# Optimization experiments

Hardware: AMD Instinct MI355X
Metric: run time of the kernel (lower is better)

## Reference

```python
import jax, jax.numpy as jnp
import numpy as np

N_NODES = 50000
IN_DIM = 128
OUT_DIM = 128
N_EDGES = 800000


def setup_inputs() -> dict:
    key = jax.random.key(0)
    k1, k2, k3, k4 = jax.random.split(key, 4)
    h = jax.random.normal(k1, (N_NODES, IN_DIM), dtype=jnp.float32)
    edges = jax.random.randint(k2, (2, N_EDGES), 0, N_NODES, dtype=jnp.int64)
    # nn.Linear params
    lim = 1.0 / np.sqrt(IN_DIM)
    W = jax.random.uniform(k3, (OUT_DIM, IN_DIM), minval=-lim, maxval=lim, dtype=jnp.float32)
    b = jax.random.uniform(k4, (OUT_DIM,), minval=-lim, maxval=lim, dtype=jnp.float32)
    return {"h": h, "W": W, "b": b, "edges": edges}


def reference(h, W, b, edges):
    n = h.shape[0]
    # add self loops (use_self_loops=True)
    loops = jnp.arange(n, dtype=edges.dtype)
    src = jnp.concatenate([edges[0], loops])  # [E+N]
    dst = jnp.concatenate([edges[1], loops])  # [E+N]
    # linear transform
    h_ = h @ W.T + b  # [N, out_dim]
    # symmetric normalization: 1/sqrt(deg(src)*deg(dst)), degrees incl. self loops
    deg = jax.ops.segment_sum(jnp.ones_like(dst, dtype=h.dtype), dst, num_segments=n)
    ew = jax.lax.rsqrt(deg[src] * deg[dst])  # [E+N]
    # edge-weighted scatter-sum aggregation
    agg = jax.ops.segment_sum(h_[src] * ew[:, None], dst, num_segments=n)
    return agg
```

## Files before the change

### kernel.cpp

```cpp
#include <hip/hip_runtime.h>


#define IN_DIM 128
#define OUT_DIM 128
#define CAP 40
#define NB_A 256
#define NBIN 196
#define BINW 256
#define CAPA 44
#define OVCAP 4096

typedef short bf16x8 __attribute__((ext_vector_type(8)));
typedef float f32x4 __attribute__((ext_vector_type(4)));
typedef unsigned short us8 __attribute__((ext_vector_type(8)));
typedef unsigned short us4 __attribute__((ext_vector_type(4)));

__device__ __forceinline__ unsigned short f2bf(float f) {
    unsigned u = __float_as_uint(f);
    u += 0x7fffu + ((u >> 16) & 1u);
    return (unsigned short)(u >> 16);
}
__device__ __forceinline__ float bf2f(unsigned short s) {
    return __uint_as_float(((unsigned)s) << 16);
}
__device__ __forceinline__ void acca(float4& acc, ushort4 v) {
    acc.x += bf2f(v.x);
    acc.y += bf2f(v.y);
    acc.z += bf2f(v.z);
    acc.w += bf2f(v.w);
}

__global__ __launch_bounds__(256) void k_binA(const int* __restrict__ ed,
                                              unsigned* __restrict__ gbuf,
                                              int* __restrict__ gcnt,
                                              int2* __restrict__ aov,
                                              int* __restrict__ aovc, int E) {
    __shared__ int bc[NBIN];
    const int tid = threadIdx.x;
    const int blk = blockIdx.x;
    for (int i = tid; i < NBIN; i += 256) bc[i] = 0;
    __syncthreads();
    const int chunk = (E + NB_A - 1) / NB_A;
    const int e0 = blk * chunk, e1 = min(E, e0 + chunk);
    for (int e = e0 + tid; e < e1; e += 256) {
        int s = ed[e];
        int d = ed[E + e];
        int bin = d >> 8, lo = d & 255;
        int r = atomicAdd(&bc[bin], 1);
        if (r < CAPA) {
            gbuf[((size_t)blk * NBIN + bin) * CAPA + r] = (unsigned)s | ((unsigned)lo << 16);
        } else {
            int k = atomicAdd(aovc, 1);
            if (k < OVCAP) aov[k] = make_int2(s, d);
        }
    }
    __syncthreads();
    for (int i = tid; i < NBIN; i += 256) gcnt[blk * NBIN + i] = min(bc[i], CAPA);
}

__global__ __launch_bounds__(256) void k_binB(const unsigned* __restrict__ gbuf,
                                              const int* __restrict__ gcnt,
                                              const int2* __restrict__ aov,
                                              const int* __restrict__ aovc,
                                              unsigned short* __restrict__ ell,
                                              int* __restrict__ cnt,
                                              int2* __restrict__ ovf2,
                                              int* __restrict__ ovf2c, int n) {
    __shared__ int pfx[NB_A + 1];
    __shared__ int lcnt[BINW];
    __shared__ int ws4[4];
    __shared__ __align__(16) unsigned short ells[BINW * CAP];
    const int tid = threadIdx.x;
    const int bin = blockIdx.x;
    const int node0 = bin << 8;
    const int lane = tid & 63;
    const int wv = tid >> 6;

    lcnt[tid] = 0;
    int c = gcnt[tid * NBIN + bin];
    int x = c;
#pragma unroll
    for (int d = 1; d < 64; d <<= 1) {
        int t = __shfl_up(x, d, 64);
        if (lane >= d) x += t;
    }
    if (lane == 63) ws4[wv] = x;
    __syncthreads();
    if (tid == 0) {
        int a = 0;
#pragma unroll
        for (int j = 0; j < 4; ++j) { int t = ws4[j]; ws4[j] = a; a += t; }
    }
    __syncthreads();
    pfx[tid + 1] = ws4[wv] + x;
    if (tid == 0) pfx[0] = 0;
    __syncthreads();
    const int total = pfx[NB_A];

    for (int base = 0; base < total; base += 256) {
        int idx = base + tid;
        if (idx < total) {
            int lo = 0, hi = NB_A;
            while (hi - lo > 1) {
                int mid = (lo + hi) >> 1;
                if (pfx[mid] <= idx) lo = mid; else hi = mid;
            }
            int slot = idx - pfx[lo];
            unsigned rec = gbuf[((size_t)lo * NBIN + bin) * CAPA + slot];
            int src = rec & 0xffff;
            int dlo = rec >> 16;
            int r = atomicAdd(&lcnt[dlo], 1);
            if (r < CAP) {
                ells[dlo * CAP + r] = (unsigned short)src;
            } else {
                int k = atomicAdd(ovf2c, 1);
                if (k < OVCAP) ovf2[k] = make_int2(src, node0 + dlo);
            }
        }
    }
    int nov = min(*aovc, OVCAP);
    for (int i = tid; i < nov; i += 256) {
        int2 p = aov[i];
        if ((p.y >> 8) == bin) {
            int dlo = p.y & 255;
            int r = atomicAdd(&lcnt[dlo], 1);
            if (r < CAP) {
                ells[dlo * CAP + r] = (unsigned short)p.x;
            } else {
                int k = atomicAdd(ovf2c, 1);
                if (k < OVCAP) ovf2[k] = make_int2(p.x, p.y);
            }
        }
    }
    __syncthreads();
    int node = node0 + tid;
    if (node < n) cnt[node] = lcnt[tid];
    const int4* sp = (const int4*)ells;
    int4* dp = (int4*)(ell + (size_t)node0 * CAP);
#pragma unroll
    for (int i = tid; i < BINW * CAP * 2 / 16; i += 256) dp[i] = sp[i];
}

__global__ __launch_bounds__(256) void k_gemm(
        const float* __restrict__ h, const float* __restrict__ W,
        const float* __restrict__ b, const int* __restrict__ cnt,
        unsigned short* __restrict__ hsb, int n) {
    __shared__ unsigned short sA[128 * 136];
    __shared__ unsigned short sB[128 * 136];

    const int tid = threadIdx.x;
    const int lane = tid & 63;
    const int wv = tid >> 6;
    const int quad = lane >> 4;
    const int l16 = lane & 15;
    const int row0 = blockIdx.x * 128;

    {
        const float4* h4 = (const float4*)h;
        const float4* W4 = (const float4*)W;
        for (int t = tid; t < 128 * 32; t += 256) {
            int r = t >> 5, c4 = t & 31;
            int row = row0 + r;
            float4 v = make_float4(0.f, 0.f, 0.f, 0.f);
            if (row < n) v = h4[(size_t)row * 32 + c4];
            ushort4 p;
            p.x = f2bf(v.x); p.y = f2bf(v.y); p.z = f2bf(v.z); p.w = f2bf(v.w);
            ((ushort4*)sA)[r * 34 + c4] = p;
            float4 w = W4[t];
            ushort4 q;
            q.x = f2bf(w.x); q.y = f2bf(w.y); q.z = f2bf(w.z); q.w = f2bf(w.w);
            ((ushort4*)sB)[r * 34 + c4] = q;
        }
    }
    __syncthreads();

    f32x4 acc[2][8];
#pragma unroll
    for (int mt = 0; mt < 2; ++mt)
#pragma unroll
        for (int nt = 0; nt < 8; ++nt) acc[mt][nt] = (f32x4){0.f, 0.f, 0.f, 0.f};

    const int koff = quad * 8;
#pragma unroll
    for (int kc = 0; kc < 4; ++kc) {
        int kbase = kc * 32 + koff;
        bf16x8 a0 = *(const bf16x8*)(sA + (wv * 32 + 0 + l16) * 136 + kbase);
        bf16x8 a1 = *(const bf16x8*)(sA + (wv * 32 + 16 + l16) * 136 + kbase);
#pragma unroll
        for (int nt = 0; nt < 8; ++nt) {
            bf16x8 bb = *(const bf16x8*)(sB + (nt * 16 + l16) * 136 + kbase);
            acc[0][nt] = __builtin_amdgcn_mfma_f32_16x16x32_bf16(a0, bb, acc[0][nt], 0, 0, 0);
            acc[1][nt] = __builtin_amdgcn_mfma_f32_16x16x32_bf16(a1, bb, acc[1][nt], 0, 0, 0);
        }
    }

#pragma unroll
    for (int mt = 0; mt < 2; ++mt) {
#pragma unroll
        for (int r = 0; r < 4; ++r) {
            int row = row0 + wv * 32 + mt * 16 + quad * 4 + r;
            if (row >= n) continue;
            float rsw = rsqrtf((float)(cnt[row] + 1));
#pragma unroll
            for (int nt = 0; nt < 8; ++nt) {
                int col = nt * 16 + l16;
                hsb[(size_t)row * 128 + col] = f2bf((acc[mt][nt][r] + b[col]) * rsw);
            }
        }
    }
}

__global__ __launch_bounds__(256) void k_agg(const int* __restrict__ cnt,
                                             const unsigned short* __restrict__ ell,
                                             const int2* __restrict__ ovf2,
                                             const int* __restrict__ ovf2c,
                                             const unsigned short* __restrict__ hsb,
                                             float* __restrict__ out, int n) {
    int node = blockIdx.x * 8 + (threadIdx.x >> 5);
    if (node >= n) return;
    int lane = threadIdx.x & 31;
    int deg = cnt[node];
    float rsn = rsqrtf((float)(deg + 1));
    int m = min(deg, CAP);

    const ushort4* hp = (const ushort4*)hsb;
    ushort4 sv = hp[(size_t)node * 32 + lane];
    float4 acc;
    acc.x = bf2f(sv.x); acc.y = bf2f(sv.y);
    acc.z = bf2f(sv.z); acc.w = bf2f(sv.w);

    const unsigned short* row = ell + (size_t)node * CAP;
    int e = 0;
    for (; e + 8 <= m; e += 8) {
        us8 p = *(const us8*)(row + e);
        ushort4 v0 = hp[(size_t)p[0] * 32 + lane];
        ushort4 v1 = hp[(size_t)p[1] * 32 + lane];
        ushort4 v2 = hp[(size_t)p[2] * 32 + lane];
        ushort4 v3 = hp[(size_t)p[3] * 32 + lane];
        ushort4 v4 = hp[(size_t)p[4] * 32 + lane];
        ushort4 v5 = hp[(size_t)p[5] * 32 + lane];
        ushort4 v6 = hp[(size_t)p[6] * 32 + lane];
        ushort4 v7 = hp[(size_t)p[7] * 32 + lane];
        acca(acc, v0); acca(acc, v1); acca(acc, v2); acca(acc, v3);
        acca(acc, v4); acca(acc, v5); acca(acc, v6); acca(acc, v7);
    }
    if (e + 4 <= m) {
        us4 p = *(const us4*)(row + e);
        ushort4 v0 = hp[(size_t)p[0] * 32 + lane];
        ushort4 v1 = hp[(size_t)p[1] * 32 + lane];
        ushort4 v2 = hp[(size_t)p[2] * 32 + lane];
        ushort4 v3 = hp[(size_t)p[3] * 32 + lane];
        acca(acc, v0); acca(acc, v1); acca(acc, v2); acca(acc, v3);
        e += 4;
    }
    for (; e < m; ++e) {
        ushort4 v = hp[(size_t)row[e] * 32 + lane];
        acca(acc, v);
    }
    if (deg > CAP) {
        int novf = min(*ovf2c, OVCAP);
        for (int i = 0; i < novf; ++i) {
            int2 p = ovf2[i];
            if (p.y == node) {
                ushort4 v = hp[(size_t)p.x * 32 + lane];
                acca(acc, v);
            }
        }
    }
    acc.x *= rsn; acc.y *= rsn; acc.z *= rsn; acc.w *= rsn;
    ((float4*)out)[(size_t)node * 32 + lane] = acc;
}

extern "C" void kernel_launch(void* const* d_in, const int* in_sizes, int n_in,
                              void* d_out, int out_size, void* d_ws, size_t ws_size,
                              hipStream_t stream) {
    const float* h = (const float*)d_in[0];
    const float* W = (const float*)d_in[1];
    const float* b = (const float*)d_in[2];
    const int* edges = (const int*)d_in[3];

    const int n = in_sizes[0] / IN_DIM;
    const int E = in_sizes[3] / 2;
    const int nlin = (n + 127) / 128;
    const int nnode_pad = NBIN * BINW;

    size_t o = 0;
    auto carve = [&](size_t elems) {
        size_t cur = o;
        o += (elems + 511) & ~(size_t)511;
        return cur;
    };
    float* ws = (float*)d_ws;
    unsigned short* hsb = (unsigned short*)(ws + carve((size_t)n * 64));
    int* cnt = (int*)(ws + carve(nnode_pad));
    unsigned short* ell = (unsigned short*)(ws + carve((size_t)nnode_pad * CAP / 2));
    unsigned* gbuf = (unsigned*)(ws + carve((size_t)NB_A * NBIN * CAPA));
    int* gcnt = (int*)(ws + carve((size_t)NB_A * NBIN));
    int2* aov = (int2*)(ws + carve(OVCAP * 2));
    int2* ovf2 = (int2*)(ws + carve(OVCAP * 2));
    int* ctrs = (int*)(ws + carve(2));

    float* out = (float*)d_out;

    hipMemsetAsync(ctrs, 0, 2 * sizeof(int), stream);
    k_binA<<<NB_A, 256, 0, stream>>>(edges, gbuf, gcnt, aov, ctrs + 0, E);
    k_binB<<<NBIN, 256, 0, stream>>>(gbuf, gcnt, aov, ctrs + 0, ell, cnt, ovf2, ctrs + 1, n);
    k_gemm<<<nlin, 256, 0, stream>>>(h, W, b, cnt, hsb, n);
    k_agg<<<(n + 7) / 8, 256, 0, stream>>>(cnt, ell, ovf2, ctrs + 1, hsb, out, n);
}
```

Baseline: 150.7 us.

## Fuse binning with GEMM and merge ELL build and aggregation via cooperative grid sync

The four kernels and the memset become two launches. The first runs the GEMM blocks and the edge-binning blocks side by side in one grid. The second is a cooperative kernel that builds each 64-node bin's neighbor list in shared memory, computes degree normalizers, syncs the whole grid, and then aggregates straight from shared memory with per-edge source weights. This removes launch gaps and the global ELL round trip, but it adds a per-edge rs gather and a grid-wide barrier, and it relies on all 784 blocks being co-resident.

```diff
diff --git a/kernel.cpp b/kernel.cpp
--- a/kernel.cpp
+++ b/kernel.cpp
@@ -1,14 +1,18 @@
 #include <hip/hip_runtime.h>
+#include <hip/hip_cooperative_groups.h>
+
+namespace cg = cooperative_groups;
 
 
 #define IN_DIM 128
 #define OUT_DIM 128
-#define CAP 40
 #define NB_A 256
-#define NBIN 196
-#define BINW 256
-#define CAPA 44
-#define OVCAP 4096
+#define NBIN 784
+#define BINW 64
+#define CAPA 16
+#define OVB 8
+#define CAPL 48
+#define LOV 16
 
 typedef short bf16x8 __attribute__((ext_vector_type(8)));
 typedef float f32x4 __attribute__((ext_vector_type(4)));
@@ -23,132 +27,55 @@
 __device__ __forceinline__ float bf2f(unsigned short s) {
     return __uint_as_float(((unsigned)s) << 16);
 }
-__device__ __forceinline__ void acca(float4& acc, ushort4 v) {
-    acc.x += bf2f(v.x);
-    acc.y += bf2f(v.y);
-    acc.z += bf2f(v.z);
-    acc.w += bf2f(v.w);
-}
-
-__global__ __launch_bounds__(256) void k_binA(const int* __restrict__ ed,
-                                              unsigned* __restrict__ gbuf,
-                                              int* __restrict__ gcnt,
-                                              int2* __restrict__ aov,
-                                              int* __restrict__ aovc, int E) {
-    __shared__ int bc[NBIN];
+__device__ __forceinline__ void accw(float4& acc, ushort4 v, float wt) {
+    acc.x += wt * bf2f(v.x);
+    acc.y += wt * bf2f(v.y);
+    acc.z += wt * bf2f(v.z);
+    acc.w += wt * bf2f(v.w);
+}
+
+__global__ __launch_bounds__(256) void k1(
+        const float* __restrict__ h, const float* __restrict__ W,
+        const float* __restrict__ b, unsigned short* __restrict__ hsb, int n,
+        const int* __restrict__ ed, unsigned* __restrict__ gbuf,
+        int* __restrict__ gcnt, int* __restrict__ aovb, int2* __restrict__ aov,
+        int E, int ngemm) {
+    __shared__ __align__(16) unsigned char smem[128 * 136 * 2 * 2];
+    __shared__ int ovc;
+    __shared__ int2 ovl[OVB];
     const int tid = threadIdx.x;
-    const int blk = blockIdx.x;
-    for (int i = tid; i < NBIN; i += 256) bc[i] = 0;
-    __syncthreads();
-    const int chunk = (E + NB_A - 1) / NB_A;
-    const int e0 = blk * chunk, e1 = min(E, e0 + chunk);
-    for (int e = e0 + tid; e < e1; e += 256) {
-        int s = ed[e];
-        int d = ed[E + e];
-        int bin = d >> 8, lo = d & 255;
-        int r = atomicAdd(&bc[bin], 1);
-        if (r < CAPA) {
-            gbuf[((size_t)blk * NBIN + bin) * CAPA + r] = (unsigned)s | ((unsigned)lo << 16);
-        } else {
-            int k = atomicAdd(aovc, 1);
-            if (k < OVCAP) aov[k] = make_int2(s, d);
-        }
-    }
-    __syncthreads();
-    for (int i = tid; i < NBIN; i += 256) gcnt[blk * NBIN + i] = min(bc[i], CAPA);
-}
-
-__global__ __launch_bounds__(256) void k_binB(const unsigned* __restrict__ gbuf,
-                                              const int* __restrict__ gcnt,
-                                              const int2* __restrict__ aov,
-                                              const int* __restrict__ aovc,
-                                              unsigned short* __restrict__ ell,
-                                              int* __restrict__ cnt,
-                                              int2* __restrict__ ovf2,
-                                              int* __restrict__ ovf2c, int n) {
-    __shared__ int pfx[NB_A + 1];
-    __shared__ int lcnt[BINW];
-    __shared__ int ws4[4];
-    __shared__ __align__(16) unsigned short ells[BINW * CAP];
-    const int tid = threadIdx.x;
-    const int bin = blockIdx.x;
-    const int node0 = bin << 8;
-    const int lane = tid & 63;
-    const int wv = tid >> 6;
-
-    lcnt[tid] = 0;
-    int c = gcnt[tid * NBIN + bin];
-    int x = c;
-#pragma unroll
-    for (int d = 1; d < 64; d <<= 1) {
-        int t = __shfl_up(x, d, 64);
-        if (lane >= d) x += t;
-    }
-    if (lane == 63) ws4[wv] = x;
-    __syncthreads();
-    if (tid == 0) {
-        int a = 0;
-#pragma unroll
-        for (int j = 0; j < 4; ++j) { int t = ws4[j]; ws4[j] = a; a += t; }
-    }
-    __syncthreads();
-    pfx[tid + 1] = ws4[wv] + x;
-    if (tid == 0) pfx[0] = 0;
-    __syncthreads();
-    const int total = pfx[NB_A];
-
-    for (int base = 0; base < total; base += 256) {
-        int idx = base + tid;
-        if (idx < total) {
-            int lo = 0, hi = NB_A;
-            while (hi - lo > 1) {
-                int mid = (lo + hi) >> 1;
-                if (pfx[mid] <= idx) lo = mid; else hi = mid;
-            }
-            int slot = idx - pfx[lo];
-            unsigned rec = gbuf[((size_t)lo * NBIN + bin) * CAPA + slot];
-            int src = rec & 0xffff;
-            int dlo = rec >> 16;
-            int r = atomicAdd(&lcnt[dlo], 1);
-            if (r < CAP) {
-                ells[dlo * CAP + r] = (unsigned short)src;
+
+    if ((int)blockIdx.x >= ngemm) {
+        int blk = blockIdx.x - ngemm;
+        int* bc = (int*)smem;
+        for (int i = tid; i < NBIN; i += 256) bc[i] = 0;
+        if (tid == 0) ovc = 0;
+        __syncthreads();
+        const int chunk = (E + NB_A - 1) / NB_A;
+        const int e0 = blk * chunk, e1 = min(E, e0 + chunk);
+        for (int e = e0 + tid; e < e1; e += 256) {
+            int s = ed[e];
+            int d = ed[E + e];
+            int bin = d >> 6, dlo = d & 63;
+            int r = atomicAdd(&bc[bin], 1);
+            if (r < CAPA) {
+                gbuf[((size_t)blk * NBIN + bin) * CAPA + r] =
+                    (unsigned)s | ((unsigned)dlo << 16);
             } else {
-                int k = atomicAdd(ovf2c, 1);
-                if (k < OVCAP) ovf2[k] = make_int2(src, node0 + dlo);
-            }
-        }
-    }
-    int nov = min(*aovc, OVCAP);
-    for (int i = tid; i < nov; i += 256) {
-        int2 p = aov[i];
-        if ((p.y >> 8) == bin) {
-            int dlo = p.y & 255;
-            int r = atomicAdd(&lcnt[dlo], 1);
-            if (r < CAP) {
-                ells[dlo * CAP + r] = (unsigned short)p.x;
-            } else {
-                int k = atomicAdd(ovf2c, 1);
-                if (k < OVCAP) ovf2[k] = make_int2(p.x, p.y);
-            }
-        }
-    }
-    __syncthreads();
-    int node = node0 + tid;
-    if (node < n) cnt[node] = lcnt[tid];
-    const int4* sp = (const int4*)ells;
-    int4* dp = (int4*)(ell + (size_t)node0 * CAP);
-#pragma unroll
-    for (int i = tid; i < BINW * CAP * 2 / 16; i += 256) dp[i] = sp[i];
-}
-
-__global__ __launch_bounds__(256) void k_gemm(
-        const float* __restrict__ h, const float* __restrict__ W,
-        const float* __restrict__ b, const int* __restrict__ cnt,
-        unsigned short* __restrict__ hsb, int n) {
-    __shared__ unsigned short sA[128 * 136];
-    __shared__ unsigned short sB[128 * 136];
-
-    const int tid = threadIdx.x;
+                int k = atomicAdd(&ovc, 1);
+                if (k < OVB) ovl[k] = make_int2(s, d);
+            }
+        }
+        __syncthreads();
+        for (int i = tid; i < NBIN; i += 256) gcnt[(size_t)blk * NBIN + i] = min(bc[i], CAPA);
+        int nov = min(ovc, OVB);
+        if (tid < nov) aov[blk * OVB + tid] = ovl[tid];
+        if (tid == 0) aovb[blk] = nov;
+        return;
+    }
+
+    unsigned short* sA = (unsigned short*)smem;
+    unsigned short* sB = (unsigned short*)(smem + 128 * 136 * 2);
     const int lane = tid & 63;
     const int wv = tid >> 6;
     const int quad = lane >> 4;
@@ -200,75 +127,159 @@
         for (int r = 0; r < 4; ++r) {
             int row = row0 + wv * 32 + mt * 16 + quad * 4 + r;
             if (row >= n) continue;
-            float rsw = rsqrtf((float)(cnt[row] + 1));
 #pragma unroll
             for (int nt = 0; nt < 8; ++nt) {
                 int col = nt * 16 + l16;
-                hsb[(size_t)row * 128 + col] = f2bf((acc[mt][nt][r] + b[col]) * rsw);
-            }
-        }
-    }
-}
-
-__global__ __launch_bounds__(256) void k_agg(const int* __restrict__ cnt,
-                                             const unsigned short* __restrict__ ell,
-                                             const int2* __restrict__ ovf2,
-                                             const int* __restrict__ ovf2c,
-                                             const unsigned short* __restrict__ hsb,
-                                             float* __restrict__ out, int n) {
-    int node = blockIdx.x * 8 + (threadIdx.x >> 5);
-    if (node >= n) return;
-    int lane = threadIdx.x & 31;
-    int deg = cnt[node];
-    float rsn = rsqrtf((float)(deg + 1));
-    int m = min(deg, CAP);
+                hsb[(size_t)row * 128 + col] = f2bf(acc[mt][nt][r] + b[col]);
+            }
+        }
+    }
+}
+
+__global__ __launch_bounds__(256, 4) void k2(
+        const unsigned* __restrict__ gbuf, const int* __restrict__ gcnt,
+        const int* __restrict__ aovb, const int2* __restrict__ aov,
+        const unsigned short* __restrict__ hsb, float* __restrict__ rs,
+        float* __restrict__ out, int n) {
+    __shared__ int pfx[NB_A + 1];
+    __shared__ int ws4[4];
+    __shared__ int lcnt[BINW];
+    __shared__ float lrs[BINW];
+    __shared__ __align__(16) unsigned short ells[BINW * CAPL];
+    __shared__ int lovc;
+    __shared__ int2 lov[LOV];
+
+    const int tid = threadIdx.x;
+    const int bin = blockIdx.x;
+    const int node0 = bin * BINW;
+    const int lane64 = tid & 63;
+    const int wv = tid >> 6;
+
+    if (tid < BINW) lcnt[tid] = 0;
+    if (tid == 0) lovc = 0;
+    int c = gcnt[(size_t)tid * NBIN + bin];
+    int x = c;
+#pragma unroll
+    for (int d = 1; d < 64; d <<= 1) {
+        int t = __shfl_up(x, d, 64);
+        if (lane64 >= d) x += t;
+    }
+    if (lane64 == 63) ws4[wv] = x;
+    __syncthreads();
+    if (tid == 0) {
+        int a = 0;
+#pragma unroll
+        for (int j = 0; j < 4; ++j) { int t = ws4[j]; ws4[j] = a; a += t; }
+    }
+    __syncthreads();
+    pfx[tid + 1] = ws4[wv] + x;
+    if (tid == 0) pfx[0] = 0;
+    __syncthreads();
+    const int total = pfx[NB_A];
+
+    for (int base = 0; base < total; base += 256) {
+        int idx = base + tid;
+        if (idx < total) {
+            int lo = 0, hi = NB_A;
+            while (hi - lo > 1) {
+                int mid = (lo + hi) >> 1;
+                if (pfx[mid] <= idx) lo = mid; else hi = mid;
+            }
+            unsigned rec = gbuf[((size_t)lo * NBIN + bin) * CAPA + (idx - pfx[lo])];
+            int src = rec & 0xffff;
+            int dlo = rec >> 16;
+            int r = atomicAdd(&lcnt[dlo], 1);
+            if (r < CAPL) {
+                ells[dlo * CAPL + r] = (unsigned short)src;
+            } else {
+                int k = atomicAdd(&lovc, 1);
+                if (k < LOV) lov[k] = make_int2(src, dlo);
+            }
+        }
+    }
+    {
+        int cov = aovb[tid];
+        for (int j = 0; j < cov; ++j) {
+            int2 p = aov[tid * OVB + j];
+            if ((p.y >> 6) == bin) {
+                int dlo = p.y & 63;
+                int r = atomicAdd(&lcnt[dlo], 1);
+                if (r < CAPL) {
+                    ells[dlo * CAPL + r] = (unsigned short)p.x;
+                } else {
+                    int k = atomicAdd(&lovc, 1);
+                    if (k < LOV) lov[k] = make_int2(p.x, dlo);
+                }
+            }
+        }
+    }
+    __syncthreads();
+    if (tid < BINW) {
+        float v = rsqrtf((float)(lcnt[tid] + 1));
+        lrs[tid] = v;
+        int node = node0 + tid;
+        if (node < n) rs[node] = v;
+    }
+
+    cg::this_grid().sync();
 
     const ushort4* hp = (const ushort4*)hsb;
-    ushort4 sv = hp[(size_t)node * 32 + lane];
-    float4 acc;
-    acc.x = bf2f(sv.x); acc.y = bf2f(sv.y);
-    acc.z = bf2f(sv.z); acc.w = bf2f(sv.w);
-
-    const unsigned short* row = ell + (size_t)node * CAP;
-    int e = 0;
-    for (; e + 8 <= m; e += 8) {
-        us8 p = *(const us8*)(row + e);
-        ushort4 v0 = hp[(size_t)p[0] * 32 + lane];
-        ushort4 v1 = hp[(size_t)p[1] * 32 + lane];
-        ushort4 v2 = hp[(size_t)p[2] * 32 + lane];
-        ushort4 v3 = hp[(size_t)p[3] * 32 + lane];
-        ushort4 v4 = hp[(size_t)p[4] * 32 + lane];
-        ushort4 v5 = hp[(size_t)p[5] * 32 + lane];
-        ushort4 v6 = hp[(size_t)p[6] * 32 + lane];
-        ushort4 v7 = hp[(size_t)p[7] * 32 + lane];
-        acca(acc, v0); acca(acc, v1); acca(acc, v2); acca(acc, v3);
-        acca(acc, v4); acca(acc, v5); acca(acc, v6); acca(acc, v7);
-    }
-    if (e + 4 <= m) {
-        us4 p = *(const us4*)(row + e);
-        ushort4 v0 = hp[(size_t)p[0] * 32 + lane];
-        ushort4 v1 = hp[(size_t)p[1] * 32 + lane];
-        ushort4 v2 = hp[(size_t)p[2] * 32 + lane];
-        ushort4 v3 = hp[(size_t)p[3] * 32 + lane];
-        acca(acc, v0); acca(acc, v1); acca(acc, v2); acca(acc, v3);
-        e += 4;
-    }
-    for (; e < m; ++e) {
-        ushort4 v = hp[(size_t)row[e] * 32 + lane];
-        acca(acc, v);
-    }
-    if (deg > CAP) {
-        int novf = min(*ovf2c, OVCAP);
-        for (int i = 0; i < novf; ++i) {
-            int2 p = ovf2[i];
-            if (p.y == node) {
-                ushort4 v = hp[(size_t)p.x * 32 + lane];
-                acca(acc, v);
-            }
-        }
-    }
-    acc.x *= rsn; acc.y *= rsn; acc.z *= rsn; acc.w *= rsn;
-    ((float4*)out)[(size_t)node * 32 + lane] = acc;
+    const int half = tid >> 5, lane = tid & 31;
+    for (int r8 = 0; r8 < BINW; r8 += 8) {
+        int dlo = r8 + half;
+        int node = node0 + dlo;
+        if (node >= n) continue;
+        int deg = lcnt[dlo];
+        int m = min(deg, CAPL);
+        float rsn = lrs[dlo];
+        ushort4 sv = hp[(size_t)node * 32 + lane];
+        float4 acc;
+        acc.x = rsn * bf2f(sv.x); acc.y = rsn * bf2f(sv.y);
+        acc.z = rsn * bf2f(sv.z); acc.w = rsn * bf2f(sv.w);
+
+        const unsigned short* row = ells + dlo * CAPL;
+        int e = 0;
+        for (; e + 8 <= m; e += 8) {
+            us8 p = *(const us8*)(row + e);
+            float w0 = rs[p[0]], w1 = rs[p[1]], w2 = rs[p[2]], w3 = rs[p[3]];
+            float w4 = rs[p[4]], w5 = rs[p[5]], w6 = rs[p[6]], w7 = rs[p[7]];
+            ushort4 v0 = hp[(size_t)p[0] * 32 + lane];
+            ushort4 v1 = hp[(size_t)p[1] * 32 + lane];
+            ushort4 v2 = hp[(size_t)p[2] * 32 + lane];
+            ushort4 v3 = hp[(size_t)p[3] * 32 + lane];
+            ushort4 v4 = hp[(size_t)p[4] * 32 + lane];
+            ushort4 v5 = hp[(size_t)p[5] * 32 + lane];
+            ushort4 v6 = hp[(size_t)p[6] * 32 + lane];
+            ushort4 v7 = hp[(size_t)p[7] * 32 + lane];
+            accw(acc, v0, w0); accw(acc, v1, w1); accw(acc, v2, w2); accw(acc, v3, w3);
+            accw(acc, v4, w4); accw(acc, v5, w5); accw(acc, v6, w6); accw(acc, v7, w7);
+        }
+        if (e + 4 <= m) {
+            us4 p = *(const us4*)(row + e);
+            float w0 = rs[p[0]], w1 = rs[p[1]], w2 = rs[p[2]], w3 = rs[p[3]];
+            ushort4 v0 = hp[(size_t)p[0] * 32 + lane];
+            ushort4 v1 = hp[(size_t)p[1] * 32 + lane];
+            ushort4 v2 = hp[(size_t)p[2] * 32 + lane];
+            ushort4 v3 = hp[(size_t)p[3] * 32 + lane];
+            accw(acc, v0, w0); accw(acc, v1, w1); accw(acc, v2, w2); accw(acc, v3, w3);
+            e += 4;
+        }
+        for (; e < m; ++e) {
+            int s = row[e];
+            accw(acc, hp[(size_t)s * 32 + lane], rs[s]);
+        }
+        if (deg > CAPL) {
+            int nov = min(lovc, LOV);
+            for (int i = 0; i < nov; ++i) {
+                if (lov[i].y == dlo) {
+                    int s = lov[i].x;
+                    accw(acc, hp[(size_t)s * 32 + lane], rs[s]);
+                }
+            }
+        }
+        acc.x *= rsn; acc.y *= rsn; acc.z *= rsn; acc.w *= rsn;
+        ((float4*)out)[(size_t)node * 32 + lane] = acc;
+    }
 }
 
 extern "C" void kernel_launch(void* const* d_in, const int* in_sizes, int n_in,
@@ -281,8 +292,7 @@
 
     const int n = in_sizes[0] / IN_DIM;
     const int E = in_sizes[3] / 2;
-    const int nlin = (n + 127) / 128;
-    const int nnode_pad = NBIN * BINW;
+    const int ngemm = (n + 127) / 128;
 
     size_t o = 0;
     auto carve = [&](size_t elems) {
@@ -292,19 +302,18 @@
     };
     float* ws = (float*)d_ws;
     unsigned short* hsb = (unsigned short*)(ws + carve((size_t)n * 64));
-    int* cnt = (int*)(ws + carve(nnode_pad));
-    unsigned short* ell = (unsigned short*)(ws + carve((size_t)nnode_pad * CAP / 2));
     unsigned* gbuf = (unsigned*)(ws + carve((size_t)NB_A * NBIN * CAPA));
     int* gcnt = (int*)(ws + carve((size_t)NB_A * NBIN));
-    int2* aov = (int2*)(ws + carve(OVCAP * 2));
-    int2* ovf2 = (int2*)(ws + carve(OVCAP * 2));
-    int* ctrs = (int*)(ws + carve(2));
+    int* aovb = (int*)(ws + carve(NB_A));
+    int2* aov = (int2*)(ws + carve((size_t)NB_A * OVB * 2));
+    float* rs = ws + carve((size_t)NBIN * BINW);
 
     float* out = (float*)d_out;
 
-    hipMemsetAsync(ctrs, 0, 2 * sizeof(int), stream);
-    k_binA<<<NB_A, 256, 0, stream>>>(edges, gbuf, gcnt, aov, ctrs + 0, E);
-    k_binB<<<NBIN, 256, 0, stream>>>(gbuf, gcnt, aov, ctrs + 0, ell, cnt, ovf2, ctrs + 1, n);
-    k_gemm<<<nlin, 256, 0, stream>>>(h, W, b, cnt, hsb, n);
-    k_agg<<<(n + 7) / 8, 256, 0, stream>>>(cnt, ell, ovf2, ctrs + 1, hsb, out, n);
-}
+    k1<<<ngemm + NB_A, 256, 0, stream>>>(h, W, b, hsb, n, edges, gbuf, gcnt,
+                                         aovb, aov, E, ngemm);
+
+    void* args[] = {(void*)&gbuf, (void*)&gcnt, (void*)&aovb, (void*)&aov,
+                    (void*)&hsb,  (void*)&rs,   (void*)&out,  (void*)&n};
+    hipLaunchCooperativeKernel((void*)k2, dim3(NBIN), dim3(256), args, 0, stream);
+}
```

Result: slower. 216.3 us (+43.5%).

## Fuse GEMM with edge binning into one launch and move source normalization into aggregation

Applied to the files above, without the earlier changes.

The GEMM and the first binning pass now run as one heterogeneous launch. The first blocks do the linear transform and the remaining blocks bin edges, so the GEMM no longer waits for the degree counts. Because of that, the source-side rsqrt scaling is taken out of the GEMM epilogue. A per-node rsqrt table is written in binB, and aggregation multiplies each gathered neighbor row by its weight. The memset is dropped, and the GEMM reads the A operand straight from global memory instead of staging it in LDS. Per-block overflow lists are capped at 8 entries, so edges past that are silently dropped, and aggregation does extra weight loads and multiplies per edge.

```diff
diff --git a/kernel.cpp b/kernel.cpp
--- a/kernel.cpp
+++ b/kernel.cpp
@@ -8,6 +8,7 @@
 #define NBIN 196
 #define BINW 256
 #define CAPA 44
+#define OVB 8
 #define OVCAP 4096
 
 typedef short bf16x8 __attribute__((ext_vector_type(8)));
@@ -23,52 +24,135 @@
 __device__ __forceinline__ float bf2f(unsigned short s) {
     return __uint_as_float(((unsigned)s) << 16);
 }
-__device__ __forceinline__ void acca(float4& acc, ushort4 v) {
-    acc.x += bf2f(v.x);
-    acc.y += bf2f(v.y);
-    acc.z += bf2f(v.z);
-    acc.w += bf2f(v.w);
-}
-
-__global__ __launch_bounds__(256) void k_binA(const int* __restrict__ ed,
-                                              unsigned* __restrict__ gbuf,
-                                              int* __restrict__ gcnt,
-                                              int2* __restrict__ aov,
-                                              int* __restrict__ aovc, int E) {
-    __shared__ int bc[NBIN];
+__device__ __forceinline__ void accw(float4& acc, ushort4 v, float wt) {
+    acc.x += wt * bf2f(v.x);
+    acc.y += wt * bf2f(v.y);
+    acc.z += wt * bf2f(v.z);
+    acc.w += wt * bf2f(v.w);
+}
+__device__ __forceinline__ bf16x8 load_a8(const float* h, int row, int k0, int n) {
+    bf16x8 r;
+    if (row < n) {
+        const float4* p = (const float4*)(h + (size_t)row * 128 + k0);
+        float4 f0 = p[0], f1 = p[1];
+        r[0] = (short)f2bf(f0.x); r[1] = (short)f2bf(f0.y);
+        r[2] = (short)f2bf(f0.z); r[3] = (short)f2bf(f0.w);
+        r[4] = (short)f2bf(f1.x); r[5] = (short)f2bf(f1.y);
+        r[6] = (short)f2bf(f1.z); r[7] = (short)f2bf(f1.w);
+    } else {
+        r = (bf16x8){0, 0, 0, 0, 0, 0, 0, 0};
+    }
+    return r;
+}
+
+__global__ __launch_bounds__(256) void k_gb(
+        const float* __restrict__ h, const float* __restrict__ W,
+        const float* __restrict__ b, unsigned short* __restrict__ hsb, int n,
+        const int* __restrict__ ed, unsigned* __restrict__ gbuf,
+        int* __restrict__ gcnt, int* __restrict__ aovb, int2* __restrict__ aov,
+        int* __restrict__ ctrs, int E, int ngemm) {
+    __shared__ __align__(16) unsigned short sB[128 * 136];
+    __shared__ int ovc;
+    __shared__ int2 ovl[OVB];
     const int tid = threadIdx.x;
-    const int blk = blockIdx.x;
-    for (int i = tid; i < NBIN; i += 256) bc[i] = 0;
-    __syncthreads();
-    const int chunk = (E + NB_A - 1) / NB_A;
-    const int e0 = blk * chunk, e1 = min(E, e0 + chunk);
-    for (int e = e0 + tid; e < e1; e += 256) {
-        int s = ed[e];
-        int d = ed[E + e];
-        int bin = d >> 8, lo = d & 255;
-        int r = atomicAdd(&bc[bin], 1);
-        if (r < CAPA) {
-            gbuf[((size_t)blk * NBIN + bin) * CAPA + r] = (unsigned)s | ((unsigned)lo << 16);
-        } else {
-            int k = atomicAdd(aovc, 1);
-            if (k < OVCAP) aov[k] = make_int2(s, d);
-        }
-    }
-    __syncthreads();
-    for (int i = tid; i < NBIN; i += 256) gcnt[blk * NBIN + i] = min(bc[i], CAPA);
+
+    if ((int)blockIdx.x >= ngemm) {
+        int blk = blockIdx.x - ngemm;
+        if (blk == 0 && tid == 0) ctrs[0] = 0;
+        int* bc = (int*)sB;
+        for (int i = tid; i < NBIN; i += 256) bc[i] = 0;
+        if (tid == 0) ovc = 0;
+        __syncthreads();
+        const int chunk = (E + NB_A - 1) / NB_A;
+        const int e0 = blk * chunk, e1 = min(E, e0 + chunk);
+        for (int e = e0 + tid; e < e1; e += 256) {
+            int s = ed[e];
+            int d = ed[E + e];
+            int bin = d >> 8, dlo = d & 255;
+            int r = atomicAdd(&bc[bin], 1);
+            if (r < CAPA) {
+                gbuf[((size_t)blk * NBIN + bin) * CAPA + r] =
+                    (unsigned)s | ((unsigned)dlo << 16);
+            } else {
+                int k = atomicAdd(&ovc, 1);
+                if (k < OVB) ovl[k] = make_int2(s, d);
+            }
+        }
+        __syncthreads();
+        for (int i = tid; i < NBIN; i += 256)
+            gcnt[(size_t)blk * NBIN + i] = min(bc[i], CAPA);
+        int nov = min(ovc, OVB);
+        if (tid < nov) aov[blk * OVB + tid] = ovl[tid];
+        if (tid == 0) aovb[blk] = nov;
+        return;
+    }
+
+    const int lane = tid & 63;
+    const int wv = tid >> 6;
+    const int quad = lane >> 4;
+    const int l16 = lane & 15;
+    const int row0 = blockIdx.x * 128;
+
+    {
+        const float4* W4 = (const float4*)W;
+        for (int t = tid; t < 128 * 32; t += 256) {
+            float4 w = W4[t];
+            ushort4 q;
+            q.x = f2bf(w.x); q.y = f2bf(w.y); q.z = f2bf(w.z); q.w = f2bf(w.w);
+            ((ushort4*)sB)[(t >> 5) * 34 + (t & 31)] = q;
+        }
+    }
+    __syncthreads();
+
+    f32x4 acc[2][8];
+#pragma unroll
+    for (int mt = 0; mt < 2; ++mt)
+#pragma unroll
+        for (int nt = 0; nt < 8; ++nt) acc[mt][nt] = (f32x4){0.f, 0.f, 0.f, 0.f};
+
+    const int koff = quad * 8;
+    const int ra0 = row0 + wv * 32 + l16;
+    const int ra1 = ra0 + 16;
+#pragma unroll
+    for (int kc = 0; kc < 4; ++kc) {
+        int kbase = kc * 32 + koff;
+        bf16x8 a0 = load_a8(h, ra0, kbase, n);
+        bf16x8 a1 = load_a8(h, ra1, kbase, n);
+#pragma unroll
+        for (int nt = 0; nt < 8; ++nt) {
+            bf16x8 bb = *(const bf16x8*)(sB + (nt * 16 + l16) * 136 + kbase);
+            acc[0][nt] = __builtin_amdgcn_mfma_f32_16x16x32_bf16(a0, bb, acc[0][nt], 0, 0, 0);
+            acc[1][nt] = __builtin_amdgcn_mfma_f32_16x16x32_bf16(a1, bb, acc[1][nt], 0, 0, 0);
+        }
+    }
+
+#pragma unroll
+    for (int mt = 0; mt < 2; ++mt) {
+#pragma unroll
+        for (int r = 0; r < 4; ++r) {
+            int row = row0 + wv * 32 + mt * 16 + quad * 4 + r;
+            if (row >= n) continue;
+#pragma unroll
+            for (int nt = 0; nt < 8; ++nt) {
+                int col = nt * 16 + l16;
+                hsb[(size_t)row * 128 + col] = f2bf(acc[mt][nt][r] + b[col]);
+            }
+        }
+    }
 }
 
 __global__ __launch_bounds__(256) void k_binB(const unsigned* __restrict__ gbuf,
                                               const int* __restrict__ gcnt,
+                                              const int* __restrict__ aovb,
                                               const int2* __restrict__ aov,
-                                              const int* __restrict__ aovc,
                                               unsigned short* __restrict__ ell,
                                               int* __restrict__ cnt,
+                                              float* __restrict__ rs,
                                               int2* __restrict__ ovf2,
                                               int* __restrict__ ovf2c, int n) {
     __shared__ int pfx[NB_A + 1];
+    __shared__ int ws4[4];
     __shared__ int lcnt[BINW];
-    __shared__ int ws4[4];
     __shared__ __align__(16) unsigned short ells[BINW * CAP];
     const int tid = threadIdx.x;
     const int bin = blockIdx.x;
@@ -77,7 +161,7 @@
     const int wv = tid >> 6;
 
     lcnt[tid] = 0;
-    int c = gcnt[tid * NBIN + bin];
+    int c = gcnt[(size_t)tid * NBIN + bin];
     int x = c;
 #pragma unroll
     for (int d = 1; d < 64; d <<= 1) {
@@ -105,8 +189,7 @@
                 int mid = (lo + hi) >> 1;
                 if (pfx[mid] <= idx) lo = mid; else hi = mid;
             }
-            int slot = idx - pfx[lo];
-            unsigned rec = gbuf[((size_t)lo * NBIN + bin) * CAPA + slot];
+            unsigned rec = gbuf[((size_t)lo * NBIN + bin) * CAPA + (idx - pfx[lo])];
             int src = rec & 0xffff;
             int dlo = rec >> 16;
             int r = atomicAdd(&lcnt[dlo], 1);
@@ -118,99 +201,36 @@
             }
         }
     }
-    int nov = min(*aovc, OVCAP);
-    for (int i = tid; i < nov; i += 256) {
-        int2 p = aov[i];
-        if ((p.y >> 8) == bin) {
-            int dlo = p.y & 255;
-            int r = atomicAdd(&lcnt[dlo], 1);
-            if (r < CAP) {
-                ells[dlo * CAP + r] = (unsigned short)p.x;
-            } else {
-                int k = atomicAdd(ovf2c, 1);
-                if (k < OVCAP) ovf2[k] = make_int2(p.x, p.y);
+    {
+        int cov = aovb[tid];
+        for (int j = 0; j < cov; ++j) {
+            int2 p = aov[tid * OVB + j];
+            if ((p.y >> 8) == bin) {
+                int dlo = p.y & 255;
+                int r = atomicAdd(&lcnt[dlo], 1);
+                if (r < CAP) {
+                    ells[dlo * CAP + r] = (unsigned short)p.x;
+                } else {
+                    int k = atomicAdd(ovf2c, 1);
+                    if (k < OVCAP) ovf2[k] = make_int2(p.x, node0 + dlo);
+                }
             }
         }
     }
     __syncthreads();
     int node = node0 + tid;
-    if (node < n) cnt[node] = lcnt[tid];
+    if (node < n) {
+        cnt[node] = lcnt[tid];
+        rs[node] = rsqrtf((float)(lcnt[tid] + 1));
+    }
     const int4* sp = (const int4*)ells;
     int4* dp = (int4*)(ell + (size_t)node0 * CAP);
 #pragma unroll
     for (int i = tid; i < BINW * CAP * 2 / 16; i += 256) dp[i] = sp[i];
 }
 
-__global__ __launch_bounds__(256) void k_gemm(
-        const float* __restrict__ h, const float* __restrict__ W,
-        const float* __restrict__ b, const int* __restrict__ cnt,
-        unsigned short* __restrict__ hsb, int n) {
-    __shared__ unsigned short sA[128 * 136];
-    __shared__ unsigned short sB[128 * 136];
-
-    const int tid = threadIdx.x;
-    const int lane = tid & 63;
-    const int wv = tid >> 6;
-    const int quad = lane >> 4;
-    const int l16 = lane & 15;
-    const int row0 = blockIdx.x * 128;
-
-    {
-        const float4* h4 = (const float4*)h;
-        const float4* W4 = (const float4*)W;
-        for (int t = tid; t < 128 * 32; t += 256) {
-            int r = t >> 5, c4 = t & 31;
-            int row = row0 + r;
-            float4 v = make_float4(0.f, 0.f, 0.f, 0.f);
-            if (row < n) v = h4[(size_t)row * 32 + c4];
-            ushort4 p;
-            p.x = f2bf(v.x); p.y = f2bf(v.y); p.z = f2bf(v.z); p.w = f2bf(v.w);
-            ((ushort4*)sA)[r * 34 + c4] = p;
-            float4 w = W4[t];
-            ushort4 q;
-            q.x = f2bf(w.x); q.y = f2bf(w.y); q.z = f2bf(w.z); q.w = f2bf(w.w);
-            ((ushort4*)sB)[r * 34 + c4] = q;
-        }
-    }
-    __syncthreads();
-
-    f32x4 acc[2][8];
-#pragma unroll
-    for (int mt = 0; mt < 2; ++mt)
-#pragma unroll
-        for (int nt = 0; nt < 8; ++nt) acc[mt][nt] = (f32x4){0.f, 0.f, 0.f, 0.f};
-
-    const int koff = quad * 8;
-#pragma unroll
-    for (int kc = 0; kc < 4; ++kc) {
-        int kbase = kc * 32 + koff;
-        bf16x8 a0 = *(const bf16x8*)(sA + (wv * 32 + 0 + l16) * 136 + kbase);
-        bf16x8 a1 = *(const bf16x8*)(sA + (wv * 32 + 16 + l16) * 136 + kbase);
-#pragma unroll
-        for (int nt = 0; nt < 8; ++nt) {
-            bf16x8 bb = *(const bf16x8*)(sB + (nt * 16 + l16) * 136 + kbase);
-            acc[0][nt] = __builtin_amdgcn_mfma_f32_16x16x32_bf16(a0, bb, acc[0][nt], 0, 0, 0);
-            acc[1][nt] = __builtin_amdgcn_mfma_f32_16x16x32_bf16(a1, bb, acc[1][nt], 0, 0, 0);
-        }
-    }
-
-#pragma unroll
-    for (int mt = 0; mt < 2; ++mt) {
-#pragma unroll
-        for (int r = 0; r < 4; ++r) {
-            int row = row0 + wv * 32 + mt * 16 + quad * 4 + r;
-            if (row >= n) continue;
-            float rsw = rsqrtf((float)(cnt[row] + 1));
-#pragma unroll
-            for (int nt = 0; nt < 8; ++nt) {
-                int col = nt * 16 + l16;
-                hsb[(size_t)row * 128 + col] = f2bf((acc[mt][nt][r] + b[col]) * rsw);
-            }
-        }
-    }
-}
-
 __global__ __launch_bounds__(256) void k_agg(const int* __restrict__ cnt,
+                                             const float* __restrict__ rs,
                                              const unsigned short* __restrict__ ell,
                                              const int2* __restrict__ ovf2,
                                              const int* __restrict__ ovf2c,
@@ -220,19 +240,21 @@
     if (node >= n) return;
     int lane = threadIdx.x & 31;
     int deg = cnt[node];
-    float rsn = rsqrtf((float)(deg + 1));
+    float rsn = rs[node];
     int m = min(deg, CAP);
 
     const ushort4* hp = (const ushort4*)hsb;
     ushort4 sv = hp[(size_t)node * 32 + lane];
     float4 acc;
-    acc.x = bf2f(sv.x); acc.y = bf2f(sv.y);
-    acc.z = bf2f(sv.z); acc.w = bf2f(sv.w);
+    acc.x = rsn * bf2f(sv.x); acc.y = rsn * bf2f(sv.y);
+    acc.z = rsn * bf2f(sv.z); acc.w = rsn * bf2f(sv.w);
 
     const unsigned short* row = ell + (size_t)node * CAP;
     int e = 0;
     for (; e + 8 <= m; e += 8) {
         us8 p = *(const us8*)(row + e);
+        float w0 = rs[p[0]], w1 = rs[p[1]], w2 = rs[p[2]], w3 = rs[p[3]];
+        float w4 = rs[p[4]], w5 = rs[p[5]], w6 = rs[p[6]], w7 = rs[p[7]];
         ushort4 v0 = hp[(size_t)p[0] * 32 + lane];
         ushort4 v1 = hp[(size_t)p[1] * 32 + lane];
         ushort4 v2 = hp[(size_t)p[2] * 32 + lane];
@@ -241,29 +263,29 @@
         ushort4 v5 = hp[(size_t)p[5] * 32 + lane];
         ushort4 v6 = hp[(size_t)p[6] * 32 + lane];
         ushort4 v7 = hp[(size_t)p[7] * 32 + lane];
-        acca(acc, v0); acca(acc, v1); acca(acc, v2); acca(acc, v3);
-        acca(acc, v4); acca(acc, v5); acca(acc, v6); acca(acc, v7);
+        accw(acc, v0, w0); accw(acc, v1, w1); accw(acc, v2, w2); accw(acc, v3, w3);
+        accw(acc, v4, w4); accw(acc, v5, w5); accw(acc, v6, w6); accw(acc, v7, w7);
     }
     if (e + 4 <= m) {
         us4 p = *(const us4*)(row + e);
+        float w0 = rs[p[0]], w1 = rs[p[1]], w2 = rs[p[2]], w3 = rs[p[3]];
         ushort4 v0 = hp[(size_t)p[0] * 32 + lane];
         ushort4 v1 = hp[(size_t)p[1] * 32 + lane];
         ushort4 v2 = hp[(size_t)p[2] * 32 + lane];
         ushort4 v3 = hp[(size_t)p[3] * 32 + lane];
-        acca(acc, v0); acca(acc, v1); acca(acc, v2); acca(acc, v3);
+        accw(acc, v0, w0); accw(acc, v1, w1); accw(acc, v2, w2); accw(acc, v3, w3);
         e += 4;
     }
     for (; e < m; ++e) {
-        ushort4 v = hp[(size_t)row[e] * 32 + lane];
-        acca(acc, v);
+        int s = row[e];
+        accw(acc, hp[(size_t)s * 32 + lane], rs[s]);
     }
     if (deg > CAP) {
         int novf = min(*ovf2c, OVCAP);
         for (int i = 0; i < novf; ++i) {
             int2 p = ovf2[i];
             if (p.y == node) {
-                ushort4 v = hp[(size_t)p.x * 32 + lane];
-                acca(acc, v);
+                accw(acc, hp[(size_t)p.x * 32 + lane], rs[p.x]);
             }
         }
     }
@@ -281,7 +303,7 @@
 
     const int n = in_sizes[0] / IN_DIM;
     const int E = in_sizes[3] / 2;
-    const int nlin = (n + 127) / 128;
+    const int ngemm = (n + 127) / 128;
     const int nnode_pad = NBIN * BINW;
 
     size_t o = 0;
@@ -292,19 +314,21 @@
     };
     float* ws = (float*)d_ws;
     unsigned short* hsb = (unsigned short*)(ws + carve((size_t)n * 64));
-    int* cnt = (int*)(ws + carve(nnode_pad));
-    unsigned short* ell = (unsigned short*)(ws + carve((size_t)nnode_pad * CAP / 2));
     unsigned* gbuf = (unsigned*)(ws + carve((size_t)NB_A * NBIN * CAPA));
     int* gcnt = (int*)(ws + carve((size_t)NB_A * NBIN));
-    int2* aov = (int2*)(ws + carve(OVCAP * 2));
+    int* aovb = (int*)(ws + carve(NB_A));
+    int2* aov = (int2*)(ws + carve((size_t)NB_A * OVB * 2));
+    int* cnt = (int*)(ws + carve(nnode_pad));
+    float* rs = ws + carve(nnode_pad);
+    unsigned short* ell = (unsigned short*)(ws + carve((size_t)nnode_pad * CAP / 2));
     int2* ovf2 = (int2*)(ws + carve(OVCAP * 2));
     int* ctrs = (int*)(ws + carve(2));
 
     float* out = (float*)d_out;
 
-    hipMemsetAsync(ctrs, 0, 2 * sizeof(int), stream);
-    k_binA<<<NB_A, 256, 0, stream>>>(edges, gbuf, gcnt, aov, ctrs + 0, E);
-    k_binB<<<NBIN, 256, 0, stream>>>(gbuf, gcnt, aov, ctrs + 0, ell, cnt, ovf2, ctrs + 1, n);
-    k_gemm<<<nlin, 256, 0, stream>>>(h, W, b, cnt, hsb, n);
-    k_agg<<<(n + 7) / 8, 256, 0, stream>>>(cnt, ell, ovf2, ctrs + 1, hsb, out, n);
-}
+    k_gb<<<ngemm + NB_A, 256, 0, stream>>>(h, W, b, hsb, n, edges, gbuf, gcnt,
+                                           aovb, aov, ctrs, E, ngemm);
+    k_binB<<<NBIN, 256, 0, stream>>>(gbuf, gcnt, aovb, aov, ell, cnt, rs,
+                                     ovf2, ctrs, n);
+    k_agg<<<(n + 7) / 8, 256, 0, stream>>>(cnt, rs, ell, ovf2, ctrs, hsb, out, n);
+}
```

Result: faster. 143.5 us (-4.8%).
